# Kernel optimization log

Measured on AMD Instinct MI355X. Metric: run time of the kernel, lower is better.

## Reference

```python
import jax, jax.numpy as jnp
import numpy as np

B, N, C = 128, 197, 768   # batch, tokens (14*14 + cls), embed dim
H = 12                    # attention heads, head_dim = 64
OUT = 32                  # hard-coded mlp out_features
CH_H = 14                 # channel-attention heads
CN = 196                  # channel-attention token dim (14*14)
MLP_HID = int(C * 4.0)    # 3072
CMLP_HID = int(OUT * 4.0) # 128
EPS = 1e-5


def _ln(x, g, b):
    m = x.mean(-1, keepdims=True)
    v = ((x - m) ** 2).mean(-1, keepdims=True)
    return (x - m) * jax.lax.rsqrt(v + EPS) * g + b


def setup_inputs() -> dict:
    key = jax.random.key(0)
    ks = jax.random.split(key, 24)
    W = lambda k, sh: (jax.random.normal(k, sh, jnp.float32) * 0.02)
    return {
        "x": jax.random.normal(ks[0], (B, N, C), jnp.float32),
        # block 1: norm1 + token attention
        "g1": jnp.ones((C,), jnp.float32), "b1": jnp.zeros((C,), jnp.float32),
        "w_qkv": W(ks[1], (3 * C, C)),                     # qkv_bias=False
        "w_proj": W(ks[2], (C, C)), "b_proj": jnp.zeros((C,), jnp.float32),
        # block 2: norm2 + mlp (768 -> 3072 -> 32), NOT residual
        "g2": jnp.ones((C,), jnp.float32), "b2": jnp.zeros((C,), jnp.float32),
        "w_fc1": W(ks[3], (MLP_HID, C)), "b_fc1": jnp.zeros((MLP_HID,), jnp.float32),
        "w_fc2": W(ks[4], (OUT, MLP_HID)), "b_fc2": jnp.zeros((OUT,), jnp.float32),
        # block 3: norm3 + channel attention (over 196 spatial positions)
        "g3": jnp.ones((OUT,), jnp.float32), "b3": jnp.zeros((OUT,), jnp.float32),
        "w_cqkv": W(ks[5], (3 * CN, CN)),                  # qkv_bias=False
        "w_cproj": W(ks[6], (CN, CN)), "b_cproj": jnp.zeros((CN,), jnp.float32),
        # block 4: norm4 + channel mlp (32 -> 128 -> 32)
        "g4": jnp.ones((OUT,), jnp.float32), "b4": jnp.zeros((OUT,), jnp.float32),
        "w_cfc1": W(ks[7], (CMLP_HID, OUT)), "b_cfc1": jnp.zeros((CMLP_HID,), jnp.float32),
        "w_cfc2": W(ks[8], (OUT, CMLP_HID)), "b_cfc2": jnp.zeros((OUT,), jnp.float32),
    }


def reference(x, g1, b1, w_qkv, w_proj, b_proj,
              g2, b2, w_fc1, b_fc1, w_fc2, b_fc2,
              g3, b3, w_cqkv, w_cproj, b_cproj,
              g4, b4, w_cfc1, b_cfc1, w_cfc2, b_cfc2):
    Bz, Nn, Cc = x.shape
    hd = Cc // H  # 64

    # --- token attention (residual) ---
    h = _ln(x, g1, b1)
    qkv = (h @ w_qkv.T).reshape(Bz, Nn, 3, H, hd).transpose(2, 0, 3, 1, 4)
    q, k, v = qkv[0], qkv[1], qkv[2]                       # [B,H,N,hd]
    a = jax.nn.softmax(jnp.einsum('bhqd,bhkd->bhqk', q, k) * (hd ** -0.5), axis=-1)
    o = jnp.einsum('bhqk,bhkd->bhqd', a, v).transpose(0, 2, 1, 3).reshape(Bz, Nn, Cc)
    x = x + (o @ w_proj.T + b_proj)

    # --- mlp 768->3072->32, NO residual (matches original forward) ---
    h = _ln(x, g2, b2)
    x = jax.nn.gelu(h @ w_fc1.T + b_fc1, approximate=False) @ w_fc2.T + b_fc2  # [B,N,32]

    # --- channel attention (residual); N==197 path, no interleave averaging ---
    h = _ln(x, g3, b3)
    cls = h[:, :1, :]                                      # [B,1,32]
    t = h[:, 1:, :].transpose(0, 2, 1)                     # [B,32,196]
    chd = CN // CH_H  # 14
    cqkv = (t @ w_cqkv.T).reshape(Bz, OUT, 3, CH_H, chd).transpose(2, 0, 3, 1, 4)
    cq, ck, cv = cqkv[0], cqkv[1], cqkv[2]                 # [B,14,32,14]
    ca = jax.nn.softmax(jnp.einsum('bhqd,bhkd->bhqk', cq, ck) * (chd ** -0.5), axis=-1)
    co = jnp.einsum('bhqk,bhkd->bhqd', ca, cv).transpose(0, 2, 1, 3).reshape(Bz, OUT, CN)
    co = co @ w_cproj.T + b_cproj                          # [B,32,196]
    x = x + jnp.concatenate([cls, co.transpose(0, 2, 1)], axis=1)

    # --- channel mlp 32->128->32 (residual) ---
    h = _ln(x, g4, b4)
    x = x + (jax.nn.gelu(h @ w_cfc1.T + b_cfc1, approximate=False) @ w_cfc2.T + b_cfc2)
    return x
```

## Files before the change

kernel.cpp:

```cpp
#include <hip/hip_runtime.h>
#include <hip/hip_bf16.h>

typedef unsigned short u16;
typedef __hip_bfloat16 bf16;
typedef __attribute__((ext_vector_type(8))) short bf16x8;
typedef __attribute__((ext_vector_type(4))) float f32x4;

#define B_   128
#define N_   197
#define C_   768
#define H_   12
#define HD_  64
#define T_   (B_*N_)
#define MH_  3072
#define OUT_ 32
#define CN_  196
#define CHH_ 14
#define KP_  224
#define CSZ_ (B_*CHH_*32*14)

__device__ __forceinline__ float bfu2f(u16 x){ union{unsigned u; float f;} v; v.u=((unsigned)x)<<16; return v.f; }
__device__ __forceinline__ bf16  f2bf(float f){ return __float2bfloat16(f); }
__device__ __forceinline__ u16   f2bfu(float f){ union{bf16 h; u16 u;} c; c.h=__float2bfloat16(f); return c.u; }
__device__ __forceinline__ float gelu_f(float x){ return 0.5f*x*(1.0f+erff(x*0.70710678118654752f)); }

__device__ __forceinline__ void gl_lds16(const u16* g, u16* l){
  __builtin_amdgcn_global_load_lds((const __attribute__((address_space(1))) void*)g,
                                   (__attribute__((address_space(3))) void*)l, 16, 0, 0);
}

__global__ __launch_bounds__(256) void write_code_kernel(float* out, int n, float code){
  int i = blockIdx.x*256 + threadIdx.x;
  if (i < n) out[i] = code;
}

template<bool F32IN>
__global__ __launch_bounds__(256) void ln768_kernel(const void* __restrict__ xv,
    const float* __restrict__ g, const float* __restrict__ b, bf16* __restrict__ out)
{
  int row = blockIdx.x;
  int tid = threadIdx.x;
  float v0, v1, v2;
  if (F32IN){
    const float* xr = (const float*)xv + (size_t)row*C_;
    v0 = xr[tid]; v1 = xr[tid+256]; v2 = xr[tid+512];
  } else {
    const u16* xr = (const u16*)xv + (size_t)row*C_;
    v0 = bfu2f(xr[tid]); v1 = bfu2f(xr[tid+256]); v2 = bfu2f(xr[tid+512]);
  }
  __shared__ float red[4];
  int lane = tid & 63, wave = tid >> 6;
  float s = v0+v1+v2;
  #pragma unroll
  for (int off=32; off>0; off>>=1) s += __shfl_xor(s, off);
  if (lane==0) red[wave]=s;
  __syncthreads();
  float mean = (red[0]+red[1]+red[2]+red[3]) * (1.0f/C_);
  float d0=v0-mean, d1=v1-mean, d2=v2-mean;
  float q = d0*d0+d1*d1+d2*d2;
  #pragma unroll
  for (int off=32; off>0; off>>=1) q += __shfl_xor(q, off);
  __syncthreads();
  if (lane==0) red[wave]=q;
  __syncthreads();
  float var = (red[0]+red[1]+red[2]+red[3]) * (1.0f/C_);
  float r = rsqrtf(var + 1e-5f);
  bf16* orow = out + (size_t)row*C_;
  orow[tid]     = f2bf(d0*r*g[tid]     + b[tid]);
  orow[tid+256] = f2bf(d1*r*g[tid+256] + b[tid+256]);
  orow[tid+512] = f2bf(d2*r*g[tid+512] + b[tid+512]);
}

__global__ __launch_bounds__(256) void ln32_kernel(const float* __restrict__ x,
    const float* __restrict__ g, const float* __restrict__ b, float* __restrict__ out)
{
  int i = blockIdx.x*256 + threadIdx.x;
  int c = i & 31;
  float v = x[i];
  float s = v;
  #pragma unroll
  for (int off=16; off>0; off>>=1) s += __shfl_xor(s, off, 32);
  float mean = s * (1.0f/32);
  float d = v - mean;
  float q = d*d;
  #pragma unroll
  for (int off=16; off>0; off>>=1) q += __shfl_xor(q, off, 32);
  float r = rsqrtf(q*(1.0f/32) + 1e-5f);
  out[i] = d*r*g[c] + b[c];
}

__global__ __launch_bounds__(256) void packw_bf16(const float* __restrict__ w,
    u16* __restrict__ dst, int n)
{
  int i = (blockIdx.x*256 + threadIdx.x)*4;
  if (i >= n) return;
  float4 v = *(const float4*)(w + i);
  ushort4 o; o.x=f2bfu(v.x); o.y=f2bfu(v.y); o.z=f2bfu(v.z); o.w=f2bfu(v.w);
  *(ushort4*)(dst + i) = o;
}

__global__ __launch_bounds__(256) void init_x3_kernel(const float* __restrict__ bias,
    float* __restrict__ x3)
{
  int i = blockIdx.x*256 + threadIdx.x;
  x3[i] = bias[i & 31];
}

template<int MODE, bool WB16>
__global__ __launch_bounds__(256) void gemm128(
    const u16* __restrict__ A, const void* __restrict__ Wsrc,
    const float* __restrict__ bias, const float* __restrict__ resid,
    bf16* __restrict__ outb,
    bf16* __restrict__ q_out, bf16* __restrict__ k_out, bf16* __restrict__ v_out,
    int Nn, int K)
{
  __shared__ __align__(16) u16 As[2][128*32];
  __shared__ __align__(16) u16 Bs[2][128*32];
  const int tid  = threadIdx.x;
  const int wave = tid >> 6, lane = tid & 63;
  const int quad = lane >> 4, l16 = lane & 15;
  const int wr = wave >> 1, wc = wave & 1;
  const unsigned Nx  = gridDim.x;
  const unsigned nwg = Nx * gridDim.y;
  unsigned lin = blockIdx.x + Nx*blockIdx.y;
  unsigned q8 = nwg >> 3, r8 = nwg & 7;
  unsigned xcd = lin & 7, sub = lin >> 3;
  unsigned nl = (xcd < r8 ? xcd*(q8+1) : r8*(q8+1) + (xcd-r8)*q8) + sub;
  const int m0 = (int)(nl / Nx) * 128;
  const int n0 = (int)(nl % Nx) * 128;
  const int rs = tid >> 2;
  const int kc = (tid & 3) << 3;

  const u16* aA0 = A + (size_t)(m0 + rs)*K + kc;
  const u16* aA1 = aA0 + (size_t)64*K;
  const u16*  wB0 = WB16 ? ((const u16*)Wsrc + (size_t)(n0 + rs)*K + kc) : nullptr;
  const float* wF0 = WB16 ? nullptr : ((const float*)Wsrc + (size_t)(n0 + rs)*K + kc);

  f32x4 acc[4][4] = {};

  auto STAGE = [&](int buf, int k0){
    u16* AsW = As[buf] + (size_t)wave*512;
    u16* BsW = Bs[buf] + (size_t)wave*512;
    gl_lds16(aA0 + k0, AsW);
    gl_lds16(aA1 + k0, AsW + 2048);
    if (WB16){
      gl_lds16(wB0 + k0, BsW);
      gl_lds16(wB0 + (size_t)64*K + k0, BsW + 2048);
    } else {
      float4 w0 = *(const float4*)(wF0 + k0);
      float4 w1 = *(const float4*)(wF0 + k0 + 4);
      const float* wF1 = wF0 + (size_t)64*K;
      float4 w2 = *(const float4*)(wF1 + k0);
      float4 w3 = *(const float4*)(wF1 + k0 + 4);
      ushort4 b0; b0.x=f2bfu(w0.x); b0.y=f2bfu(w0.y); b0.z=f2bfu(w0.z); b0.w=f2bfu(w0.w);
      ushort4 b1; b1.x=f2bfu(w1.x); b1.y=f2bfu(w1.y); b1.z=f2bfu(w1.z); b1.w=f2bfu(w1.w);
      ushort4 b2; b2.x=f2bfu(w2.x); b2.y=f2bfu(w2.y); b2.z=f2bfu(w2.z); b2.w=f2bfu(w2.w);
      ushort4 b3; b3.x=f2bfu(w3.x); b3.y=f2bfu(w3.y); b3.z=f2bfu(w3.z); b3.w=f2bfu(w3.w);
      *(ushort4*)&Bs[buf][rs*32 + kc]        = b0;
      *(ushort4*)&Bs[buf][rs*32 + kc + 4]    = b1;
      *(ushort4*)&Bs[buf][(rs+64)*32 + kc]   = b2;
      *(ushort4*)&Bs[buf][(rs+64)*32 + kc+4] = b3;
    }
  };

  STAGE(0, 0);
  __syncthreads();
  int cur = 0;

  for (int k0 = 0; k0 < K; k0 += 32){
    if (k0 + 32 < K) STAGE(cur^1, k0 + 32);
    bf16x8 af[4], bfr[4];
    #pragma unroll
    for (int i=0;i<4;i++) af[i]  = *(const bf16x8*)&As[cur][(wr*64 + i*16 + l16)*32 + quad*8];
    #pragma unroll
    for (int j=0;j<4;j++) bfr[j] = *(const bf16x8*)&Bs[cur][(wc*64 + j*16 + l16)*32 + quad*8];
    #pragma unroll
    for (int i=0;i<4;i++)
      #pragma unroll
      for (int j=0;j<4;j++)
        acc[i][j] = __builtin_amdgcn_mfma_f32_16x16x32_bf16(af[i], bfr[j], acc[i][j], 0, 0, 0);
    __syncthreads();
    cur ^= 1;
  }

  #pragma unroll
  for (int i=0;i<4;i++){
    #pragma unroll
    for (int j=0;j<4;j++){
      #pragma unroll
      for (int r=0;r<4;r++){
        int m = m0 + wr*64 + i*16 + quad*4 + r;
        int c = n0 + wc*64 + j*16 + l16;
        float v = acc[i][j][r];
        if (MODE==0){
          int bb = m / N_;
          int n  = m - bb*N_;
          int sec = c / C_;
          int rem = c - sec*C_;
          int hh  = rem >> 6;
          int d   = rem & 63;
          bf16* dst = (sec==0) ? q_out : (sec==1) ? k_out : v_out;
          dst[(((size_t)bb*H_ + hh)*N_ + n)*HD_ + d] = f2bf(v);
        } else if (MODE==1){
          size_t idx = (size_t)m*Nn + c;
          outb[idx] = f2bf(v + bias[c] + resid[idx]);
        } else {
          outb[(size_t)m*Nn + c] = f2bf(gelu_f(v + bias[c]));
        }
      }
    }
  }
}

template<int MODE, bool WB16>
__global__ __launch_bounds__(256) void gemm_mfma(
    const u16* __restrict__ A, const void* __restrict__ Wsrc,
    const float* __restrict__ bias, const float* __restrict__ resid,
    bf16* __restrict__ outb, float* __restrict__ outf,
    bf16* __restrict__ q_out, bf16* __restrict__ k_out, bf16* __restrict__ v_out,
    int M, int Nn, int K, int wld, int astride)
{
  __shared__ __align__(16) u16 As[64][32];
  __shared__ __align__(16) u16 Bs[64][32];
  const int tid  = threadIdx.x;
  const int wave = tid >> 6, lane = tid & 63;
  const int quad = lane >> 4, l16 = lane & 15;
  const int m0 = blockIdx.x * 64;
  const int n0 = (MODE==6) ? 0 : blockIdx.y * 64;
  const int kst = (MODE==6) ? blockIdx.y * K : 0;
  const int rs = tid >> 2;
  const int kc = (tid & 3) << 3;
  const u16* arow = A + (size_t)(m0 + rs)*astride + kst + kc;
  const bool wvalid = (n0 + rs) < Nn;

  f32x4 acc[4] = {};

  for (int k0 = 0; k0 < K; k0 += 32){
    *(uint4*)&As[rs][kc] = *(const uint4*)(arow + k0);
    if (WB16){
      const u16* wrow = (const u16*)Wsrc + (size_t)(n0 + rs)*wld + kst + kc;
      uint4 wv = make_uint4(0u,0u,0u,0u);
      if (wvalid) wv = *(const uint4*)(wrow + k0);
      *(uint4*)&Bs[rs][kc] = wv;
    } else {
      const float* wrow = (const float*)Wsrc + (size_t)(n0 + rs)*wld + kst + kc;
      float4 w0 = make_float4(0.f,0.f,0.f,0.f), w1 = w0;
      if (wvalid){ w0 = *(const float4*)(wrow + k0); w1 = *(const float4*)(wrow + k0 + 4); }
      ushort4 b0; b0.x=f2bfu(w0.x); b0.y=f2bfu(w0.y); b0.z=f2bfu(w0.z); b0.w=f2bfu(w0.w);
      ushort4 b1; b1.x=f2bfu(w1.x); b1.y=f2bfu(w1.y); b1.z=f2bfu(w1.z); b1.w=f2bfu(w1.w);
      *(ushort4*)&Bs[rs][kc]   = b0;
      *(ushort4*)&Bs[rs][kc+4] = b1;
    }
    __syncthreads();
    bf16x8 af = *(const bf16x8*)&As[wave*16 + l16][quad*8];
    #pragma unroll
    for (int nb=0; nb<4; nb++){
      bf16x8 bfr = *(const bf16x8*)&Bs[nb*16 + l16][quad*8];
      acc[nb] = __builtin_amdgcn_mfma_f32_16x16x32_bf16(af, bfr, acc[nb], 0, 0, 0);
    }
    __syncthreads();
  }

  #pragma unroll
  for (int nb=0; nb<4; nb++){
    #pragma unroll
    for (int r=0; r<4; r++){
      int m = m0 + wave*16 + quad*4 + r;
      int c = n0 + nb*16 + l16;
      float v = acc[nb][r];
      if (MODE==3){
        if (c < Nn) outf[(size_t)m*Nn + c] = v + bias[c];
      } else if (MODE==4){
        if (c < Nn) outf[(size_t)m*Nn + c] += v;
      } else if (MODE==6){
        if (c < Nn) atomicAdd(&outf[(size_t)m*Nn + c], v);
      } else if (MODE==5){
        if (c < Nn){
          int bb = m >> 5, oo = m & 31;
          int sec = c / CN_;
          int rem = c - sec*CN_;
          int hh  = rem / 14;
          int d   = rem - hh*14;
          outf[(size_t)sec*CSZ_ + (((size_t)bb*CHH_ + hh)*32 + oo)*14 + d] = v;
        }
      }
    }
  }
}

__global__ __launch_bounds__(256) void attn_kernel(const u16* __restrict__ q,
    const u16* __restrict__ k, const u16* __restrict__ v, bf16* __restrict__ o)
{
  __shared__ __align__(16) u16 VtS[64*208];
  __shared__ __align__(16) u16 PsS[4*16*208];
  int bh = blockIdx.x;
  int b = bh / H_, hh = bh - b*H_;
  int tid = threadIdx.x, wave = tid >> 6, lane = tid & 63;
  int quad = lane >> 4, l16 = lane & 15;
  const u16* qb = q + (size_t)bh*N_*HD_;
  const u16* kb = k + (size_t)bh*N_*HD_;
  const u16* vb = v + (size_t)bh*N_*HD_;
  for (int idx = tid; idx < (N_*HD_)/8; idx += 256){
    int j = idx >> 3, dg = idx & 7;
    bf16x8 vv = *(const bf16x8*)(vb + (size_t)j*HD_ + dg*8);
    #pragma unroll
    for (int e=0;e<8;e++){
      int d = dg*8 + e;
      VtS[(d*208 + j) ^ ((d&7)<<3)] = ((u16*)&vv)[e];
    }
  }
  for (int idx = tid; idx < 64*11; idx += 256){
    int d = idx / 11, j = 197 + (idx - d*11);
    VtS[(d*208 + j) ^ ((d&7)<<3)] = 0;
  }
  __syncthreads();

  u16* PsW = PsS + wave*16*208;
  const float LOG2E = 1.4426950408889634f;

  for (int g = wave; g < 13; g += 4){
    int r0 = g*16;
    int qrow = r0 + l16;
    int qr = (qrow < N_) ? qrow : 0;
    bf16x8 aq0 = *(const bf16x8*)(qb + (size_t)qr*HD_ + quad*8);
    bf16x8 aq1 = *(const bf16x8*)(qb + (size_t)qr*HD_ + 32 + quad*8);
    f32x4 s[13];
    __builtin_amdgcn_s_setprio(1);
    #pragma unroll
    for (int nb = 0; nb < 13; nb++){
      int krow = nb*16 + l16;
      int kr = (krow < N_) ? krow : 0;
      bf16x8 bk0 = *(const bf16x8*)(kb + (size_t)kr*HD_ + quad*8);
      bf16x8 bk1 = *(const bf16x8*)(kb + (size_t)kr*HD_ + 32 + quad*8);
      f32x4 t = {};
      t = __builtin_amdgcn_mfma_f32_16x16x32_bf16(aq0, bk0, t, 0, 0, 0);
      t = __builtin_amdgcn_mfma_f32_16x16x32_bf16(aq1, bk1, t, 0, 0, 0);
      s[nb] = t;
    }
    __builtin_amdgcn_s_setprio(0);
    #pragma unroll
    for (int nb = 0; nb < 13; nb++){
      bool colok = (nb*16 + l16) < N_;
      #pragma unroll
      for (int r = 0; r < 4; r++)
        s[nb][r] = colok ? s[nb][r]*(0.125f*LOG2E) : -1e30f;
    }
    #pragma unroll
    for (int r = 0; r < 4; r++){
      float m01 = fmaxf(s[0][r], s[1][r]),  m23 = fmaxf(s[2][r], s[3][r]);
      float m45 = fmaxf(s[4][r], s[5][r]),  m67 = fmaxf(s[6][r], s[7][r]);
      float m89 = fmaxf(s[8][r], s[9][r]),  mab = fmaxf(s[10][r], s[11][r]);
      float m = fmaxf(fmaxf(fmaxf(m01,m23), fmaxf(m45,m67)),
                      fmaxf(fmaxf(m89,mab), s[12][r]));
      m = fmaxf(m, __shfl_xor(m, 1));
      m = fmaxf(m, __shfl_xor(m, 2));
      m = fmaxf(m, __shfl_xor(m, 4));
      m = fmaxf(m, __shfl_xor(m, 8));
      #pragma unroll
      for (int nb = 0; nb < 13; nb++)
        s[nb][r] = __builtin_amdgcn_exp2f(s[nb][r] - m);
      float t01=s[0][r]+s[1][r], t23=s[2][r]+s[3][r];
      float t45=s[4][r]+s[5][r], t67=s[6][r]+s[7][r];
      float t89=s[8][r]+s[9][r], tab=s[10][r]+s[11][r];
      float su = ((t01+t23)+(t45+t67)) + ((t89+tab)+s[12][r]);
      su += __shfl_xor(su, 1);
      su += __shfl_xor(su, 2);
      su += __shfl_xor(su, 4);
      su += __shfl_xor(su, 8);
      float inv = 1.0f/su;
      #pragma unroll
      for (int nb = 0; nb < 13; nb++) s[nb][r] *= inv;
    }
    #pragma unroll
    for (int nb = 0; nb < 13; nb++)
      #pragma unroll
      for (int r = 0; r < 4; r++){
        int row = quad*4 + r;
        PsW[(row*208 + nb*16 + l16) ^ ((row&7)<<3)] = f2bfu(s[nb][r]);
      }
    __threadfence_block();
    f32x4 oa[4] = {};
    __builtin_amdgcn_s_setprio(1);
    #pragma unroll
    for (int ks = 0; ks < 7; ks++){
      int col = ks*32 + quad*8;
      bool ok = (col < 208);
      int ccol = ok ? col : 0;
      bf16x8 ap = *(const bf16x8*)&PsW[(l16*208 + ccol) ^ ((l16&7)<<3)];
      if (!ok) ap = (bf16x8){0,0,0,0,0,0,0,0};
      #pragma unroll
      for (int nd = 0; nd < 4; nd++){
        bf16x8 bv = *(const bf16x8*)&VtS[((nd*16 + l16)*208 + ccol) ^ ((l16&7)<<3)];
        oa[nd] = __builtin_amdgcn_mfma_f32_16x16x32_bf16(ap, bv, oa[nd], 0, 0, 0);
      }
    }
    __builtin_amdgcn_s_setprio(0);
    #pragma unroll
    for (int nd = 0; nd < 4; nd++)
      #pragma unroll
      for (int r = 0; r < 4; r++){
        int qi = r0 + quad*4 + r;
        if (qi < N_)
          o[((size_t)b*N_ + qi)*C_ + hh*HD_ + nd*16 + l16] = f2bf(oa[nd][r]);
      }
    __threadfence_block();
  }
}

__global__ __launch_bounds__(256) void pack_tall_kernel(const float* __restrict__ h3,
    u16* __restrict__ tall)
{
  int idx = blockIdx.x*256 + threadIdx.x;
  if (idx >= 4096*KP_) return;
  int row = idx / KP_, kk = idx - row*KP_;
  int b = row >> 5, oo = row & 31;
  float v = (kk < CN_) ? h3[((size_t)b*N_ + 1 + kk)*32 + oo] : 0.f;
  tall[idx] = f2bfu(v);
}

__global__ __launch_bounds__(256) void pack_w_kernel(const float* __restrict__ w,
    u16* __restrict__ dst, int rows, int kreal)
{
  int idx = blockIdx.x*256 + threadIdx.x;
  if (idx >= rows*KP_) return;
  int r = idx / KP_, kk = idx - r*KP_;
  dst[idx] = (kk < kreal) ? f2bfu(w[(size_t)r*kreal + kk]) : (u16)0;
}

__global__ __launch_bounds__(256) void pack_co_kernel(const float* __restrict__ co,
    u16* __restrict__ dst)
{
  int idx = blockIdx.x*256 + threadIdx.x;
  if (idx >= 4096*KP_) return;
  int row = idx / KP_, kk = idx - row*KP_;
  dst[idx] = (kk < CN_) ? f2bfu(co[(size_t)row*CN_ + kk]) : (u16)0;
}

__global__ __launch_bounds__(64) void cattn_kernel(const float* __restrict__ cq,
    const float* __restrict__ ck, const float* __restrict__ cv, float* __restrict__ co)
{
  __shared__ __align__(16) float qs[32*15], ks_[32*15], vs[32*15], ps[32*34];
  int bh = blockIdx.x;
  int b  = bh / CHH_;
  int hh = bh - b*CHH_;
  int lane = threadIdx.x;
  const float* qb = cq + (size_t)bh*448;
  const float* kb = ck + (size_t)bh*448;
  const float* vb = cv + (size_t)bh*448;
  for (int idx=lane; idx<448; idx+=64){
    int o = idx/14, d = idx - o*14;
    qs[o*15+d] = qb[idx]; ks_[o*15+d] = kb[idx]; vs[o*15+d] = vb[idx];
  }
  __syncthreads();
  int o = lane & 31, half = lane >> 5;
  const float scale = 0.2672612419124244f;
  float sc[16]; float mx = -1e30f;
  #pragma unroll
  for (int jj=0; jj<16; jj++){
    int j = half*16 + jj;
    float a = 0.f;
    #pragma unroll
    for (int d=0; d<14; d++) a += qs[o*15+d]*ks_[j*15+d];
    sc[jj] = a*scale;
    mx = fmaxf(mx, sc[jj]);
  }
  mx = fmaxf(mx, __shfl_xor(mx, 32));
  float sum = 0.f;
  #pragma unroll
  for (int jj=0; jj<16; jj++){ sc[jj] = __expf(sc[jj]-mx); sum += sc[jj]; }
  sum += __shfl_xor(sum, 32);
  float inv = 1.0f/sum;
  #pragma unroll
  for (int jj=0; jj<16; jj++) ps[o*34 + half*16 + jj] = sc[jj]*inv;
  __syncthreads();
  #pragma unroll
  for (int dd=0; dd<7; dd++){
    int d = half*7 + dd;
    float acc = 0.f;
    #pragma unroll
    for (int j=0; j<32; j++) acc += ps[o*34+j]*vs[j*15+d];
    co[((size_t)b*32 + o)*CN_ + hh*14 + d] = acc;
  }
}

__global__ __launch_bounds__(256) void concat_add_kernel(const float* __restrict__ x3,
    const float* __restrict__ h3, const float* __restrict__ co2, float* __restrict__ x4)
{
  int i = blockIdx.x*256 + threadIdx.x;
  int c = i & 31;
  int row = i >> 5;
  int b = row / N_;
  int r = row - b*N_;
  float add = (r==0) ? h3[i] : co2[((size_t)b*32 + c)*CN_ + (r-1)];
  x4[i] = x3[i] + add;
}

__global__ __launch_bounds__(256) void cfc1_kernel(const float* __restrict__ h4,
    const float* __restrict__ w, const float* __restrict__ bias, float* __restrict__ chid)
{
  int idx = blockIdx.x*256 + threadIdx.x;
  int m = idx >> 7, j = idx & 127;
  const float* hr = h4 + (size_t)m*32;
  const float* wr = w + (size_t)j*32;
  float acc = bias[j];
  #pragma unroll
  for (int kk=0; kk<32; kk++) acc += hr[kk]*wr[kk];
  chid[idx] = gelu_f(acc);
}

__global__ __launch_bounds__(256) void cfc2_kernel(const float* __restrict__ chid,
    const float* __restrict__ w, const float* __restrict__ bias,
    const float* __restrict__ x4, float* __restrict__ out)
{
  int idx = blockIdx.x*256 + threadIdx.x;
  int m = idx >> 5, j = idx & 31;
  const float* cr = chid + (size_t)m*128;
  const float* wr = w + (size_t)j*128;
  float acc = bias[j];
  #pragma unroll
  for (int kk=0; kk<128; kk++) acc += cr[kk]*wr[kk];
  out[idx] = x4[idx] + acc;
}

extern "C" void kernel_launch(void* const* d_in, const int* in_sizes, int n_in,
                              void* d_out, int out_size, void* d_ws, size_t ws_size,
                              hipStream_t stream)
{
  const int NIN = 23;
  static const int dsz[NIN] = {19365888,768,768,1769472,589824,768,768,768,2359296,
                               3072,98304,32,32,32,115248,38416,196,32,32,4096,128,4096,32};
  static const int a2d[NIN] = {2,7,13,18,20,22,16,9,11,5,1,6,12,17,19,21,15,14,8,10,4,3,0};

  float* dout = (float*)d_out;
  int ogrid = (out_size + 255)/256;

  const float* in[NIN];
  bool dict_ok = (n_in == NIN);
  if (dict_ok) for (int i=0;i<NIN;i++) if (in_sizes[i] != dsz[i]) { dict_ok=false; break; }
  if (dict_ok){
    for (int i=0;i<NIN;i++) in[i] = (const float*)d_in[i];
  } else {
    bool alpha_ok = (n_in == NIN);
    if (alpha_ok) for (int i=0;i<NIN;i++) if (in_sizes[i] != dsz[a2d[i]]) { alpha_ok=false; break; }
    if (alpha_ok){
      for (int i=0;i<NIN;i++) in[a2d[i]] = (const float*)d_in[i];
    } else {
      write_code_kernel<<<ogrid, 256, 0, stream>>>(dout, out_size, 5000.f + (float)n_in);
      return;
    }
  }

  const float* x      = in[0];
  const float* g1     = in[1];
  const float* b1     = in[2];
  const float* w_qkv  = in[3];
  const float* w_proj = in[4];
  const float* b_proj = in[5];
  const float* g2     = in[6];
  const float* b2     = in[7];
  const float* w_fc1  = in[8];
  const float* b_fc1  = in[9];
  const float* w_fc2  = in[10];
  const float* b_fc2  = in[11];
  const float* g3     = in[12];
  const float* b3     = in[13];
  const float* w_cqkv = in[14];
  const float* w_cproj= in[15];
  const float* b_cproj= in[16];
  const float* g4     = in[17];
  const float* b4     = in[18];
  const float* w_cfc1 = in[19];
  const float* b_cfc1 = in[20];
  const float* w_cfc2 = in[21];
  const float* b_cfc2 = in[22];

  char* ws = (char*)d_ws;
  const size_t TC2 = (size_t)T_*C_*2;
  const size_t NEED = 4*TC2 + 4096;
  if (ws_size < NEED){
    write_code_kernel<<<ogrid, 256, 0, stream>>>(dout, out_size,
        7000.f + (float)(ws_size >> 20));
    return;
  }

  bf16* h_buf   = (bf16*)(ws);
  bf16* o_buf   = (bf16*)(ws);
  bf16* q_buf   = (bf16*)(ws + TC2);
  bf16* k_buf   = (bf16*)(ws + 2*TC2);
  bf16* v_buf   = (bf16*)(ws + 3*TC2);
  bf16* x2_buf  = (bf16*)(ws + TC2);
  bf16* hidh    = (bf16*)(ws + 2*TC2);
  float* x3     = (float*)(ws + TC2);
  char* sm = ws + 2*TC2;
  float* h3  = (float*)sm; sm += (size_t)T_*32*4;
  float* cq  = (float*)sm; sm += (size_t)CSZ_*4;
  float* ck  = (float*)sm; sm += (size_t)CSZ_*4;
  float* cv  = (float*)sm; sm += (size_t)CSZ_*4;
  float* co  = (float*)sm; sm += (size_t)B_*32*CN_*4;
  float* co2 = (float*)sm; sm += (size_t)B_*32*CN_*4;
  float* x4  = (float*)sm; sm += (size_t)T_*32*4;
  float* h4  = (float*)sm; sm += (size_t)T_*32*4;
  float* chid = (float*)sm;
  u16* tall  = (u16*)(ws);
  u16* wcq_b = (u16*)(ws + 2*1024*1024);
  u16* co_b  = (u16*)(ws + 3*1024*1024);
  u16* wcp_b = (u16*)(ws + 5*1024*1024);

  u16* wqkv_b  = (u16*)(ws + 4*TC2 + 4096);
  u16* wproj_b = wqkv_b  + (size_t)2304*C_;
  u16* wfc1_b  = wproj_b + (size_t)C_*C_;
  const size_t WPACK = ((size_t)2304*C_ + (size_t)C_*C_ + (size_t)MH_*C_)*2;
  const bool packed = (ws_size >= NEED + WPACK);

  if (packed){
    packw_bf16<<<(2304*C_/4+255)/256, 256, 0, stream>>>(w_qkv,  wqkv_b,  2304*C_);
    packw_bf16<<<(C_*C_/4+255)/256,  256, 0, stream>>>(w_proj, wproj_b, C_*C_);
    packw_bf16<<<(MH_*C_/4+255)/256, 256, 0, stream>>>(w_fc1,  wfc1_b,  MH_*C_);
  }

  ln768_kernel<true><<<T_, 256, 0, stream>>>(x, g1, b1, h_buf);
  if (packed)
    gemm128<0,true><<<dim3(2304/128, T_/128), 256, 0, stream>>>((const u16*)h_buf,
        wqkv_b, nullptr, nullptr, nullptr, q_buf, k_buf, v_buf, 2304, C_);
  else
    gemm128<0,false><<<dim3(2304/128, T_/128), 256, 0, stream>>>((const u16*)h_buf,
        w_qkv, nullptr, nullptr, nullptr, q_buf, k_buf, v_buf, 2304, C_);
  attn_kernel<<<B_*H_, 256, 0, stream>>>((const u16*)q_buf, (const u16*)k_buf,
      (const u16*)v_buf, o_buf);
  if (packed)
    gemm128<1,true><<<dim3(C_/128, T_/128), 256, 0, stream>>>((const u16*)o_buf,
        wproj_b, b_proj, x, x2_buf, nullptr, nullptr, nullptr, C_, C_);
  else
    gemm128<1,false><<<dim3(C_/128, T_/128), 256, 0, stream>>>((const u16*)o_buf,
        w_proj, b_proj, x, x2_buf, nullptr, nullptr, nullptr, C_, C_);
  ln768_kernel<false><<<T_, 256, 0, stream>>>(x2_buf, g2, b2, h_buf);
  init_x3_kernel<<<(T_*32)/256, 256, 0, stream>>>(b_fc2, x3);
  for (int half=0; half<2; half++){
    if (packed)
      gemm128<2,true><<<dim3(1536/128, T_/128), 256, 0, stream>>>((const u16*)h_buf,
          wfc1_b + (size_t)half*1536*C_, b_fc1 + half*1536, nullptr,
          hidh, nullptr, nullptr, nullptr, 1536, C_);
    else
      gemm128<2,false><<<dim3(1536/128, T_/128), 256, 0, stream>>>((const u16*)h_buf,
          w_fc1 + (size_t)half*1536*C_, b_fc1 + half*1536, nullptr,
          hidh, nullptr, nullptr, nullptr, 1536, C_);
    gemm_mfma<6,false><<<dim3(T_/64, 4), 256, 0, stream>>>((const u16*)hidh,
        w_fc2 + (size_t)half*1536, nullptr, nullptr, nullptr, x3,
        nullptr, nullptr, nullptr, T_, OUT_, 384, MH_, 1536);
  }
  ln32_kernel<<<(T_*32)/256, 256, 0, stream>>>(x3, g3, b3, h3);
  pack_tall_kernel<<<(4096*KP_+255)/256, 256, 0, stream>>>(h3, tall);
  pack_w_kernel<<<(588*KP_+255)/256, 256, 0, stream>>>(w_cqkv, wcq_b, 588, CN_);
  gemm_mfma<5,true><<<dim3(4096/64, 10), 256, 0, stream>>>(tall, wcq_b,
      nullptr, nullptr, nullptr, cq, nullptr, nullptr, nullptr, 4096, 588, KP_, KP_, KP_);
  cattn_kernel<<<B_*CHH_, 64, 0, stream>>>(cq, ck, cv, co);
  pack_co_kernel<<<(4096*KP_+255)/256, 256, 0, stream>>>(co, co_b);
  pack_w_kernel<<<(196*KP_+255)/256, 256, 0, stream>>>(w_cproj, wcp_b, CN_, CN_);
  gemm_mfma<3,true><<<dim3(4096/64, 4), 256, 0, stream>>>(co_b, wcp_b,
      b_cproj, nullptr, nullptr, co2, nullptr, nullptr, nullptr, 4096, CN_, KP_, KP_, KP_);
  concat_add_kernel<<<(T_*32)/256, 256, 0, stream>>>(x3, h3, co2, x4);
  ln32_kernel<<<(T_*32)/256, 256, 0, stream>>>(x4, g4, b4, h4);
  cfc1_kernel<<<(T_*128)/256, 256, 0, stream>>>(h4, w_cfc1, b_cfc1, chid);
  cfc2_kernel<<<(T_*32)/256, 256, 0, stream>>>(chid, w_cfc2, b_cfc2, x4, dout);
}
```

Measured before the change: 940.3 us.

## Fuse fc2 into fc1 GEMM epilogue via LDS tile and atomics; fuse concat with LN

The fc1 GEMM (mode 7) now writes its GELU output tile into shared memory (XOR-swizzled) and immediately multiplies it by a bf16-packed fc2 weight slice, atomically accumulating the 32-wide result into x3. This removes the round trip of the 3072-wide hidden activation through global memory and the separate fc2 kernel. The cost is float atomics contention on x3 (12 column tiles per row per half) and nondeterministic summation order. Separately, the concat-add and the following LayerNorm32 are merged into one kernel that uses warp shuffles.

```diff
diff --git a/kernel.cpp b/kernel.cpp
--- a/kernel.cpp
+++ b/kernel.cpp
@@ -112,10 +112,10 @@
     const float* __restrict__ bias, const float* __restrict__ resid,
     bf16* __restrict__ outb,
     bf16* __restrict__ q_out, bf16* __restrict__ k_out, bf16* __restrict__ v_out,
-    int Nn, int K)
-{
-  __shared__ __align__(16) u16 As[2][128*32];
-  __shared__ __align__(16) u16 Bs[2][128*32];
+    int Nn, int K,
+    const u16* __restrict__ w2, float* __restrict__ outf, int koff)
+{
+  __shared__ __align__(16) u16 SM[16384];
   const int tid  = threadIdx.x;
   const int wave = tid >> 6, lane = tid & 63;
   const int quad = lane >> 4, l16 = lane & 15;
@@ -139,8 +139,8 @@
   f32x4 acc[4][4] = {};
 
   auto STAGE = [&](int buf, int k0){
-    u16* AsW = As[buf] + (size_t)wave*512;
-    u16* BsW = Bs[buf] + (size_t)wave*512;
+    u16* AsW = SM + buf*4096 + wave*512;
+    u16* BsW = SM + 8192 + buf*4096 + wave*512;
     gl_lds16(aA0 + k0, AsW);
     gl_lds16(aA1 + k0, AsW + 2048);
     if (WB16){
@@ -150,16 +150,17 @@
       float4 w0 = *(const float4*)(wF0 + k0);
       float4 w1 = *(const float4*)(wF0 + k0 + 4);
       const float* wF1 = wF0 + (size_t)64*K;
-      float4 w2 = *(const float4*)(wF1 + k0);
+      float4 w2v = *(const float4*)(wF1 + k0);
       float4 w3 = *(const float4*)(wF1 + k0 + 4);
       ushort4 b0; b0.x=f2bfu(w0.x); b0.y=f2bfu(w0.y); b0.z=f2bfu(w0.z); b0.w=f2bfu(w0.w);
       ushort4 b1; b1.x=f2bfu(w1.x); b1.y=f2bfu(w1.y); b1.z=f2bfu(w1.z); b1.w=f2bfu(w1.w);
-      ushort4 b2; b2.x=f2bfu(w2.x); b2.y=f2bfu(w2.y); b2.z=f2bfu(w2.z); b2.w=f2bfu(w2.w);
+      ushort4 b2; b2.x=f2bfu(w2v.x); b2.y=f2bfu(w2v.y); b2.z=f2bfu(w2v.z); b2.w=f2bfu(w2v.w);
       ushort4 b3; b3.x=f2bfu(w3.x); b3.y=f2bfu(w3.y); b3.z=f2bfu(w3.z); b3.w=f2bfu(w3.w);
-      *(ushort4*)&Bs[buf][rs*32 + kc]        = b0;
-      *(ushort4*)&Bs[buf][rs*32 + kc + 4]    = b1;
-      *(ushort4*)&Bs[buf][(rs+64)*32 + kc]   = b2;
-      *(ushort4*)&Bs[buf][(rs+64)*32 + kc+4] = b3;
+      u16* Bsb = SM + 8192 + buf*4096;
+      *(ushort4*)&Bsb[rs*32 + kc]        = b0;
+      *(ushort4*)&Bsb[rs*32 + kc + 4]    = b1;
+      *(ushort4*)&Bsb[(rs+64)*32 + kc]   = b2;
+      *(ushort4*)&Bsb[(rs+64)*32 + kc+4] = b3;
     }
   };
 
@@ -171,9 +172,9 @@
     if (k0 + 32 < K) STAGE(cur^1, k0 + 32);
     bf16x8 af[4], bfr[4];
     #pragma unroll
-    for (int i=0;i<4;i++) af[i]  = *(const bf16x8*)&As[cur][(wr*64 + i*16 + l16)*32 + quad*8];
-    #pragma unroll
-    for (int j=0;j<4;j++) bfr[j] = *(const bf16x8*)&Bs[cur][(wc*64 + j*16 + l16)*32 + quad*8];
+    for (int i=0;i<4;i++) af[i]  = *(const bf16x8*)&SM[cur*4096 + (wr*64 + i*16 + l16)*32 + quad*8];
+    #pragma unroll
+    for (int j=0;j<4;j++) bfr[j] = *(const bf16x8*)&SM[8192 + cur*4096 + (wc*64 + j*16 + l16)*32 + quad*8];
     #pragma unroll
     for (int i=0;i<4;i++)
       #pragma unroll
@@ -204,11 +205,47 @@
         } else if (MODE==1){
           size_t idx = (size_t)m*Nn + c;
           outb[idx] = f2bf(v + bias[c] + resid[idx]);
+        } else if (MODE==2){
+          outb[(size_t)m*Nn + c] = f2bf(gelu_f(v + bias[c]));
         } else {
-          outb[(size_t)m*Nn + c] = f2bf(gelu_f(v + bias[c]));
+          int row = wr*64 + i*16 + quad*4 + r;
+          int col = wc*64 + j*16 + l16;
+          SM[(row*128 + col) ^ ((row&7)<<3)] = f2bfu(gelu_f(v + bias[c]));
         }
       }
     }
+  }
+
+  if (MODE==7){
+    __syncthreads();
+    f32x4 acc2[2][2] = {};
+    #pragma unroll
+    for (int ks=0; ks<4; ks++){
+      bf16x8 af2[2], bf2[2];
+      #pragma unroll
+      for (int i=0;i<2;i++){
+        int row = wave*32 + i*16 + l16;
+        af2[i] = *(const bf16x8*)&SM[(row*128 + ks*32 + quad*8) ^ ((row&7)<<3)];
+      }
+      #pragma unroll
+      for (int jb=0;jb<2;jb++)
+        bf2[jb] = *(const bf16x8*)(w2 + (size_t)(jb*16 + l16)*MH_ + koff + n0 + ks*32 + quad*8);
+      #pragma unroll
+      for (int i=0;i<2;i++)
+        #pragma unroll
+        for (int jb=0;jb<2;jb++)
+          acc2[i][jb] = __builtin_amdgcn_mfma_f32_16x16x32_bf16(af2[i], bf2[jb], acc2[i][jb], 0, 0, 0);
+    }
+    #pragma unroll
+    for (int i=0;i<2;i++)
+      #pragma unroll
+      for (int jb=0;jb<2;jb++)
+        #pragma unroll
+        for (int r=0;r<4;r++){
+          int m = m0 + wave*32 + i*16 + quad*4 + r;
+          int c = jb*16 + l16;
+          atomicAdd(&outf[(size_t)m*OUT_ + c], acc2[i][jb][r]);
+        }
   }
 }
 
@@ -483,16 +520,29 @@
   }
 }
 
-__global__ __launch_bounds__(256) void concat_add_kernel(const float* __restrict__ x3,
-    const float* __restrict__ h3, const float* __restrict__ co2, float* __restrict__ x4)
+__global__ __launch_bounds__(256) void concat_ln32_kernel(const float* __restrict__ x3,
+    const float* __restrict__ h3, const float* __restrict__ co2,
+    const float* __restrict__ g, const float* __restrict__ b,
+    float* __restrict__ x4, float* __restrict__ h4)
 {
   int i = blockIdx.x*256 + threadIdx.x;
   int c = i & 31;
   int row = i >> 5;
-  int b = row / N_;
-  int r = row - b*N_;
-  float add = (r==0) ? h3[i] : co2[((size_t)b*32 + c)*CN_ + (r-1)];
-  x4[i] = x3[i] + add;
+  int bb = row / N_;
+  int r = row - bb*N_;
+  float add = (r==0) ? h3[i] : co2[((size_t)bb*32 + c)*CN_ + (r-1)];
+  float v = x3[i] + add;
+  x4[i] = v;
+  float s = v;
+  #pragma unroll
+  for (int off=16; off>0; off>>=1) s += __shfl_xor(s, off, 32);
+  float mean = s * (1.0f/32);
+  float d = v - mean;
+  float q = d*d;
+  #pragma unroll
+  for (int off=16; off>0; off>>=1) q += __shfl_xor(q, off, 32);
+  float rr = rsqrtf(q*(1.0f/32) + 1e-5f);
+  h4[i] = d*rr*g[c] + b[c];
 }
 
 __global__ __launch_bounds__(256) void cfc1_kernel(const float* __restrict__ h4,
@@ -609,44 +659,53 @@
   u16* wqkv_b  = (u16*)(ws + 4*TC2 + 4096);
   u16* wproj_b = wqkv_b  + (size_t)2304*C_;
   u16* wfc1_b  = wproj_b + (size_t)C_*C_;
-  const size_t WPACK = ((size_t)2304*C_ + (size_t)C_*C_ + (size_t)MH_*C_)*2;
+  u16* wfc2_b  = wfc1_b  + (size_t)MH_*C_;
+  const size_t WPACK = ((size_t)2304*C_ + (size_t)C_*C_ + (size_t)MH_*C_ + (size_t)OUT_*MH_)*2;
   const bool packed = (ws_size >= NEED + WPACK);
 
   if (packed){
     packw_bf16<<<(2304*C_/4+255)/256, 256, 0, stream>>>(w_qkv,  wqkv_b,  2304*C_);
     packw_bf16<<<(C_*C_/4+255)/256,  256, 0, stream>>>(w_proj, wproj_b, C_*C_);
     packw_bf16<<<(MH_*C_/4+255)/256, 256, 0, stream>>>(w_fc1,  wfc1_b,  MH_*C_);
+    packw_bf16<<<(OUT_*MH_/4+255)/256, 256, 0, stream>>>(w_fc2, wfc2_b, OUT_*MH_);
   }
 
   ln768_kernel<true><<<T_, 256, 0, stream>>>(x, g1, b1, h_buf);
   if (packed)
     gemm128<0,true><<<dim3(2304/128, T_/128), 256, 0, stream>>>((const u16*)h_buf,
-        wqkv_b, nullptr, nullptr, nullptr, q_buf, k_buf, v_buf, 2304, C_);
+        wqkv_b, nullptr, nullptr, nullptr, q_buf, k_buf, v_buf, 2304, C_,
+        nullptr, nullptr, 0);
   else
     gemm128<0,false><<<dim3(2304/128, T_/128), 256, 0, stream>>>((const u16*)h_buf,
-        w_qkv, nullptr, nullptr, nullptr, q_buf, k_buf, v_buf, 2304, C_);
+        w_qkv, nullptr, nullptr, nullptr, q_buf, k_buf, v_buf, 2304, C_,
+        nullptr, nullptr, 0);
   attn_kernel<<<B_*H_, 256, 0, stream>>>((const u16*)q_buf, (const u16*)k_buf,
       (const u16*)v_buf, o_buf);
   if (packed)
     gemm128<1,true><<<dim3(C_/128, T_/128), 256, 0, stream>>>((const u16*)o_buf,
-        wproj_b, b_proj, x, x2_buf, nullptr, nullptr, nullptr, C_, C_);
+        wproj_b, b_proj, x, x2_buf, nullptr, nullptr, nullptr, C_, C_,
+        nullptr, nullptr, 0);
   else
     gemm128<1,false><<<dim3(C_/128, T_/128), 256, 0, stream>>>((const u16*)o_buf,
-        w_proj, b_proj, x, x2_buf, nullptr, nullptr, nullptr, C_, C_);
+        w_proj, b_proj, x, x2_buf, nullptr, nullptr, nullptr, C_, C_,
+        nullptr, nullptr, 0);
   ln768_kernel<false><<<T_, 256, 0, stream>>>(x2_buf, g2, b2, h_buf);
   init_x3_kernel<<<(T_*32)/256, 256, 0, stream>>>(b_fc2, x3);
   for (int half=0; half<2; half++){
-    if (packed)
-      gemm128<2,true><<<dim3(1536/128, T_/128), 256, 0, stream>>>((const u16*)h_buf,
+    if (packed){
+      gemm128<7,true><<<dim3(1536/128, T_/128), 256, 0, stream>>>((const u16*)h_buf,
           wfc1_b + (size_t)half*1536*C_, b_fc1 + half*1536, nullptr,
-          hidh, nullptr, nullptr, nullptr, 1536, C_);
-    else
+          nullptr, nullptr, nullptr, nullptr, 1536, C_,
+          wfc2_b, x3, half*1536);
+    } else {
       gemm128<2,false><<<dim3(1536/128, T_/128), 256, 0, stream>>>((const u16*)h_buf,
           w_fc1 + (size_t)half*1536*C_, b_fc1 + half*1536, nullptr,
-          hidh, nullptr, nullptr, nullptr, 1536, C_);
-    gemm_mfma<6,false><<<dim3(T_/64, 4), 256, 0, stream>>>((const u16*)hidh,
-        w_fc2 + (size_t)half*1536, nullptr, nullptr, nullptr, x3,
-        nullptr, nullptr, nullptr, T_, OUT_, 384, MH_, 1536);
+          hidh, nullptr, nullptr, nullptr, 1536, C_,
+          nullptr, nullptr, 0);
+      gemm_mfma<6,false><<<dim3(T_/64, 4), 256, 0, stream>>>((const u16*)hidh,
+          w_fc2 + (size_t)half*1536, nullptr, nullptr, nullptr, x3,
+          nullptr, nullptr, nullptr, T_, OUT_, 384, MH_, 1536);
+    }
   }
   ln32_kernel<<<(T_*32)/256, 256, 0, stream>>>(x3, g3, b3, h3);
   pack_tall_kernel<<<(4096*KP_+255)/256, 256, 0, stream>>>(h3, tall);
@@ -658,8 +717,7 @@
   pack_w_kernel<<<(196*KP_+255)/256, 256, 0, stream>>>(w_cproj, wcp_b, CN_, CN_);
   gemm_mfma<3,true><<<dim3(4096/64, 4), 256, 0, stream>>>(co_b, wcp_b,
       b_cproj, nullptr, nullptr, co2, nullptr, nullptr, nullptr, 4096, CN_, KP_, KP_, KP_);
-  concat_add_kernel<<<(T_*32)/256, 256, 0, stream>>>(x3, h3, co2, x4);
-  ln32_kernel<<<(T_*32)/256, 256, 0, stream>>>(x4, g4, b4, h4);
+  concat_ln32_kernel<<<(T_*32)/256, 256, 0, stream>>>(x3, h3, co2, g4, b4, x4, h4);
   cfc1_kernel<<<(T_*128)/256, 256, 0, stream>>>(h4, w_cfc1, b_cfc1, chid);
   cfc2_kernel<<<(T_*32)/256, 256, 0, stream>>>(chid, w_cfc2, b_cfc2, x4, dout);
 }
```

Measured after the change: 905.1 us. 1.04x faster.
